# Kernel tuning notes

Hardware: AMD Instinct MI355X
Metric: run time of the kernel (lower is better)

Reference implementation:

```python
import jax, jax.numpy as jnp
import numpy as np
import math

H = 8        # n_heads
FACTOR = 5   # ProbSparse factor


def layer_norm(x, g, b, eps=1e-5):
    m = x.mean(-1, keepdims=True)
    v = ((x - m) ** 2).mean(-1, keepdims=True)
    return (x - m) / jnp.sqrt(v + eps) * g + b


def conv1d_circular(x, w, b=None):
    # x: [B, L, Cin], w: [Cout, Cin, 3]; Conv1d(k=3, padding=1, padding_mode='circular')
    xp = jnp.concatenate([x[:, -1:], x, x[:, :1]], axis=1)
    y = jax.lax.conv_general_dilated(xp.transpose(0, 2, 1), w, (1,), 'VALID',
                                     dimension_numbers=('NCH', 'OIH', 'NCH'))
    if b is not None:
        y = y + b[None, :, None]
    return y.transpose(0, 2, 1)


def pos_encoding(L, d):
    pos = jnp.arange(L, dtype=jnp.float32)[:, None]
    div = jnp.exp(jnp.arange(0, d, 2, dtype=jnp.float32) * (-math.log(10000.0) / d))
    pe = jnp.zeros((L, d), dtype=jnp.float32)
    pe = pe.at[:, 0::2].set(jnp.sin(pos * div))
    pe = pe.at[:, 1::2].set(jnp.cos(pos * div))
    return pe


def prob_attention(rng, Q, K, V):
    # Q, K, V: [B, H, L, E]; non-causal ProbSparse self-attention (mask_flag=False)
    B, Hh, L, E = Q.shape
    c = FACTOR * int(np.ceil(np.log(L)))
    U_part = min(c, L)  # sampled keys per query (sparsity measurement)
    u = min(c, L)       # number of active (top) queries
    idx = jax.random.randint(rng, (L, U_part), 0, L)          # shared over B,H as in torch
    K_sample = K[:, :, idx]                                   # [B,H,L,U,E] gather
    QK_sample = jnp.einsum('bhle,bhlue->bhlu', Q, K_sample)
    M = QK_sample.max(-1) - QK_sample.sum(-1) / L             # sparsity score per query
    M_top = jax.lax.top_k(M, u)[1]                            # [B,H,u] active query ids
    Q_red = jnp.take_along_axis(Q, M_top[..., None], axis=2)  # [B,H,u,E]
    scores = jnp.einsum('bhue,bhle->bhul', Q_red, K) * (1.0 / math.sqrt(E))
    attn = jax.nn.softmax(scores, axis=-1)
    upd = jnp.einsum('bhul,bhle->bhue', attn, V)
    # initial context: mean of V for every query; overwrite active queries
    ctx = jnp.broadcast_to(V.mean(axis=2, keepdims=True), (B, Hh, L, E))
    bi = jnp.arange(B)[:, None, None]
    hi = jnp.arange(Hh)[None, :, None]
    ctx = ctx.at[bi, hi, M_top].set(upd)
    return ctx.transpose(0, 2, 1, 3)  # [B,L,H,E]


def encoder_layer(rng, x, Wq, bq, Wk, bk, Wv, bv, Wo, bo, g1, b1, w1, bf1, w2, bf2, g2, b2):
    B, L, D = x.shape
    dh = D // H
    q = (x @ Wq.T + bq).reshape(B, L, H, dh).transpose(0, 2, 1, 3)
    k = (x @ Wk.T + bk).reshape(B, L, H, dh).transpose(0, 2, 1, 3)
    v = (x @ Wv.T + bv).reshape(B, L, H, dh).transpose(0, 2, 1, 3)
    o = prob_attention(rng, q, k, v).reshape(B, L, D)
    x = x + (o @ Wo.T + bo)            # dropout is identity in eval
    x = layer_norm(x, g1, b1)
    y = jax.nn.gelu(x @ w1.T + bf1, approximate=False)  # conv1 k=1 == linear
    y = y @ w2.T + bf2
    return layer_norm(x + y, g2, b2)


def conv_distill(x, w, b, bg, bb):
    # Conv1d(circular,k=3) -> BatchNorm1d(eval: mean 0, var 1) -> ELU -> MaxPool1d(3,2,1)
    y = conv1d_circular(x, w, b)
    y = y / math.sqrt(1.0 + 1e-5) * bg + bb
    y = jax.nn.elu(y)
    yc = jnp.pad(y.transpose(0, 2, 1), ((0, 0), (0, 0), (1, 1)), constant_values=-jnp.inf)
    p = jax.lax.reduce_window(yc, -jnp.inf, jax.lax.max, (1, 1, 3), (1, 1, 2), 'VALID')
    return p.transpose(0, 2, 1)  # [B, L//2, D]


def forward(x_enc, emb_w, Wq, bq, Wk, bk, Wv, bv, Wo, bo, ln1_g, ln1_b, ff_w1, ff_b1, ff_w2, ff_b2, ln2_g, ln2_b, cv_w, cv_b, bn_g, bn_b, norm_g, norm_b):
    B, L, _ = x_enc.shape
    D = emb_w.shape[0]
    x = conv1d_circular(x_enc, emb_w) + pos_encoding(L, D)[None]  # GazeEmbedding
    base = jax.random.key(42)
    EL = Wq.shape[0]
    for i in range(EL):
        rng = jax.random.fold_in(base, i)
        x = encoder_layer(rng, x, Wq[i], bq[i], Wk[i], bk[i], Wv[i], bv[i], Wo[i], bo[i],
                          ln1_g[i], ln1_b[i], ff_w1[i], ff_b1[i], ff_w2[i], ff_b2[i], ln2_g[i], ln2_b[i])
        if i < EL - 1:
            x = conv_distill(x, cv_w[i], cv_b[i], bn_g[i], bn_b[i])
    return layer_norm(x, norm_g, norm_b)


def setup_inputs() -> dict:
    key = jax.random.key(0)
    ks = jax.random.split(key, 16)
    B, L, C, D, F, EL = 4, 2048, 2, 512, 512, 3
    s = 0.02
    return {
        'x_enc': jax.random.normal(ks[0], (B, L, C), jnp.float32),
        'emb_w': jax.random.normal(ks[1], (D, C, 3), jnp.float32) * s,
        'Wq': jax.random.normal(ks[2], (EL, D, D), jnp.float32) * s,
        'bq': jnp.zeros((EL, D), jnp.float32),
        'Wk': jax.random.normal(ks[3], (EL, D, D), jnp.float32) * s,
        'bk': jnp.zeros((EL, D), jnp.float32),
        'Wv': jax.random.normal(ks[4], (EL, D, D), jnp.float32) * s,
        'bv': jnp.zeros((EL, D), jnp.float32),
        'Wo': jax.random.normal(ks[5], (EL, D, D), jnp.float32) * s,
        'bo': jnp.zeros((EL, D), jnp.float32),
        'ln1_g': jnp.ones((EL, D), jnp.float32),
        'ln1_b': jnp.zeros((EL, D), jnp.float32),
        'ff_w1': jax.random.normal(ks[6], (EL, F, D), jnp.float32) * s,
        'ff_b1': jnp.zeros((EL, F), jnp.float32),
        'ff_w2': jax.random.normal(ks[7], (EL, D, F), jnp.float32) * s,
        'ff_b2': jnp.zeros((EL, D), jnp.float32),
        'ln2_g': jnp.ones((EL, D), jnp.float32),
        'ln2_b': jnp.zeros((EL, D), jnp.float32),
        'cv_w': jax.random.normal(ks[8], (EL - 1, D, D, 3), jnp.float32) * s,
        'cv_b': jnp.zeros((EL - 1, D), jnp.float32),
        'bn_g': jnp.ones((EL - 1, D), jnp.float32),
        'bn_b': jnp.zeros((EL - 1, D), jnp.float32),
        'norm_g': jnp.ones((D,), jnp.float32),
        'norm_b': jnp.zeros((D,), jnp.float32),
    }


def reference(x_enc, emb_w, Wq, bq, Wk, bk, Wv, bv, Wo, bo, ln1_g, ln1_b, ff_w1, ff_b1, ff_w2, ff_b2, ln2_g, ln2_b, cv_w, cv_b, bn_g, bn_b, norm_g, norm_b):
    return forward(x_enc, emb_w, Wq, bq, Wk, bk, Wv, bv, Wo, bo, ln1_g, ln1_b, ff_w1, ff_b1, ff_w2, ff_b2, ln2_g, ln2_b, cv_w, cv_b, bn_g, bn_b, norm_g, norm_b)
```

## Files before the change

### kernel.cpp

```cpp
#include <hip/hip_runtime.h>
#include <cmath>
#include <cstdint>

#define D_MODEL 512
#define NH 8
#define DH 64

static inline int ceil_div(int a, int b) { return (a + b - 1) / b; }

typedef __attribute__((ext_vector_type(8))) short short8;
typedef __attribute__((ext_vector_type(4))) float floatx4;

__device__ __forceinline__ unsigned short f2bf(float f) {
  uint32_t u = __float_as_uint(f);
  uint32_t r = (u + 0x7fffu + ((u >> 16) & 1u)) >> 16;
  return (unsigned short)r;
}
__device__ __forceinline__ float bf2f(unsigned short s) {
  return __uint_as_float(((uint32_t)s) << 16);
}

#define TF_ROTL(x, r) (((x) << (r)) | ((x) >> (32 - (r))))

__host__ __device__ inline void threefry2x32(uint32_t k0, uint32_t k1,
                                             uint32_t x0, uint32_t x1,
                                             uint32_t* o0, uint32_t* o1) {
  uint32_t ks2 = k0 ^ k1 ^ 0x1BD11BDAu;
  x0 += k0; x1 += k1;
#define TF_R4(a, b, c, d)                                    \
  x0 += x1; x1 = TF_ROTL(x1, a); x1 ^= x0;                   \
  x0 += x1; x1 = TF_ROTL(x1, b); x1 ^= x0;                   \
  x0 += x1; x1 = TF_ROTL(x1, c); x1 ^= x0;                   \
  x0 += x1; x1 = TF_ROTL(x1, d); x1 ^= x0;
  TF_R4(13, 15, 26, 6);  x0 += k1;  x1 += ks2 + 1u;
  TF_R4(17, 29, 16, 24); x0 += ks2; x1 += k0 + 2u;
  TF_R4(13, 15, 26, 6);  x0 += k0;  x1 += k1 + 3u;
  TF_R4(17, 29, 16, 24); x0 += k1;  x1 += ks2 + 4u;
  TF_R4(13, 15, 26, 6);  x0 += ks2; x1 += k0 + 5u;
#undef TF_R4
  *o0 = x0; *o1 = x1;
}

__global__ __launch_bounds__(256) void cast3_qkv_kernel(
    const float* __restrict__ s0, const float* __restrict__ s1,
    const float* __restrict__ s2, unsigned short* __restrict__ dst) {
  int sel = blockIdx.x / 768, bb = blockIdx.x % 768;
  int i = (bb * 256 + threadIdx.x) * 4;
  const float* s = (sel == 0) ? s0 : (sel == 1) ? s1 : s2;
  float4 v = *(const float4*)(s + i);
  ushort4 o;
  o.x = f2bf(v.x); o.y = f2bf(v.y); o.z = f2bf(v.z); o.w = f2bf(v.w);
  int layer = i >> 18, off = i & 262143;
  *(ushort4*)(dst + (size_t)layer * 786432 + sel * 262144 + off) = o;
}

__global__ __launch_bounds__(256) void cast3_flat_kernel(
    const float* __restrict__ s0, const float* __restrict__ s1,
    const float* __restrict__ s2, unsigned short* __restrict__ dst) {
  int sel = blockIdx.x / 768, bb = blockIdx.x % 768;
  int i = (bb * 256 + threadIdx.x) * 4;
  const float* s = (sel == 0) ? s0 : (sel == 1) ? s1 : s2;
  float4 v = *(const float4*)(s + i);
  ushort4 o;
  o.x = f2bf(v.x); o.y = f2bf(v.y); o.z = f2bf(v.z); o.w = f2bf(v.w);
  *(ushort4*)(dst + (size_t)sel * 786432 + i) = o;
}

__global__ __launch_bounds__(256) void cast_cvperm_kernel(
    const float* __restrict__ src, unsigned short* __restrict__ dst) {
  int o = blockIdx.x * 256 + threadIdx.x;
  int m = o / 786432, rem = o % 786432;
  int n = rem / 1536, q = rem % 1536;
  int k = q >> 9, c = q & 511;
  dst[o] = f2bf(src[(size_t)m * 786432 + n * 1536 + c * 3 + k]);
}

__global__ __launch_bounds__(256) void embed_kernel(
    const float* __restrict__ x_enc, const float* __restrict__ emb_w,
    float* __restrict__ x, unsigned short* __restrict__ xb, int B, int L) {
  int i = blockIdx.x * 256 + threadIdx.x;
  int total = B * L * D_MODEL;
  if (i >= total) return;
  int d = i % D_MODEL;
  int l = (i / D_MODEL) % L;
  int b = i / (D_MODEL * L);
  int lm = (l == 0) ? (L - 1) : (l - 1);
  int lp = (l == L - 1) ? 0 : (l + 1);
  const float* w = emb_w + d * 6;
  const float* xb_in = x_enc + (size_t)b * L * 2;
  float acc = 0.f;
  acc += xb_in[lm * 2 + 0] * w[0] + xb_in[l * 2 + 0] * w[1] + xb_in[lp * 2 + 0] * w[2];
  acc += xb_in[lm * 2 + 1] * w[3] + xb_in[l * 2 + 1] * w[4] + xb_in[lp * 2 + 1] * w[5];
  int j = d >> 1;
  const float coef = -0.017988946039015985f;
  float div = expf((float)(2 * j) * coef);
  float ang = (float)l * div;
  float pe = (d & 1) ? cosf(ang) : sinf(ang);
  float v = acc + pe;
  x[i] = v;
  xb[i] = f2bf(v);
}

__global__ __launch_bounds__(256) void ln_kernel(
    const float* __restrict__ in, const float* __restrict__ g,
    const float* __restrict__ b, float* __restrict__ out) {
  int row = blockIdx.x;
  int t = threadIdx.x;
  const float* xr = in + (size_t)row * D_MODEL;
  float v0 = xr[t], v1 = xr[t + 256];
  __shared__ float red[256];
  red[t] = v0 + v1;
  __syncthreads();
  for (int s = 128; s > 0; s >>= 1) { if (t < s) red[t] += red[t + s]; __syncthreads(); }
  float mean = red[0] * (1.0f / 512.0f);
  __syncthreads();
  float d0 = v0 - mean, d1 = v1 - mean;
  red[t] = d0 * d0 + d1 * d1;
  __syncthreads();
  for (int s = 128; s > 0; s >>= 1) { if (t < s) red[t] += red[t + s]; __syncthreads(); }
  float var = red[0] * (1.0f / 512.0f);
  float rstd = 1.0f / sqrtf(var + 1e-5f);
  float* outr = out + (size_t)row * D_MODEL;
  outr[t]       = d0 * rstd * g[t]       + b[t];
  outr[t + 256] = d1 * rstd * g[t + 256] + b[t + 256];
}

__global__ __launch_bounds__(256) void ln_dual_kernel(
    const float* __restrict__ in, const float* __restrict__ g,
    const float* __restrict__ b, float* __restrict__ out,
    unsigned short* __restrict__ out16) {
  int row = blockIdx.x;
  int t = threadIdx.x;
  const float* xr = in + (size_t)row * D_MODEL;
  float v0 = xr[t], v1 = xr[t + 256];
  __shared__ float red[256];
  red[t] = v0 + v1;
  __syncthreads();
  for (int s = 128; s > 0; s >>= 1) { if (t < s) red[t] += red[t + s]; __syncthreads(); }
  float mean = red[0] * (1.0f / 512.0f);
  __syncthreads();
  float d0 = v0 - mean, d1 = v1 - mean;
  red[t] = d0 * d0 + d1 * d1;
  __syncthreads();
  for (int s = 128; s > 0; s >>= 1) { if (t < s) red[t] += red[t + s]; __syncthreads(); }
  float var = red[0] * (1.0f / 512.0f);
  float rstd = 1.0f / sqrtf(var + 1e-5f);
  float* outr = out + (size_t)row * D_MODEL;
  unsigned short* o16 = out16 + (size_t)row * D_MODEL;
  float r0 = d0 * rstd * g[t] + b[t];
  float r1 = d1 * rstd * g[t + 256] + b[t + 256];
  outr[t] = r0;       o16[t] = f2bf(r0);
  outr[t + 256] = r1; o16[t + 256] = f2bf(r1);
}

__device__ __forceinline__ float epilogue_apply(int MODE, float v, float r,
                                                float g, float bb, float scl) {
  if (MODE == 1) {
    v = 0.5f * v * (1.0f + erff(v * 0.7071067811865475f));
  } else if (MODE == 2) {
    v += r;
  } else if (MODE == 3) {
    v = v * scl * g + bb;
    v = (v > 0.f) ? v : expm1f(v);
  }
  return v;
}


__device__ __forceinline__ void gload16(const void* g, void* l) {
  __builtin_amdgcn_global_load_lds(
      (const __attribute__((address_space(1))) unsigned int*)g,
      (__attribute__((address_space(3))) unsigned int*)l, 16, 0, 0);
}

__device__ __forceinline__ int xcd_swz(int orig, int nwg) {
  int q = nwg >> 3, r = nwg & 7;
  int x = orig & 7, o = orig >> 3;
  return (x < r ? x * (q + 1) : r * (q + 1) + (x - r) * q) + o;
}

__device__ __forceinline__ void stage64(const unsigned short* __restrict__ G,
                                        int ldk, int row0, int k0,
                                        unsigned short* lds, int tid) {
  const int wave = tid >> 6;
#pragma unroll
  for (int iss = 0; iss < 2; ++iss) {
    int s = iss * 256 + tid;
    int r = s >> 3;
    int cs = (s & 7) ^ (r & 7);
    gload16(G + (size_t)(row0 + r) * ldk + k0 + cs * 8,
            lds + (size_t)(iss * 256 + wave * 64) * 8);
  }
}

__device__ __forceinline__ short8 frag64(const unsigned short* t, int row,
                                         int chunk) {
  return *(const short8*)(t + row * 64 + ((chunk ^ (row & 7)) * 8));
}

struct Acc4 { floatx4 v[2][2]; };

__device__ __forceinline__ void gemm64_core(
    const unsigned short* __restrict__ A, int lda,
    const unsigned short* __restrict__ Bt, int ldb, int K, int bm, int bn,
    unsigned short* lds , int tid, Acc4& out) {
  const int wave = tid >> 6, lane = tid & 63;
  const int wm = (wave >> 1) * 32, wn = (wave & 1) * 32;
  const int quad = lane >> 4, l16 = lane & 15;
  floatx4 z = {0.f, 0.f, 0.f, 0.f};
  floatx4 a00 = z, a01 = z, a10 = z, a11 = z;
  stage64(A, lda, bm, 0, lds, tid);
  stage64(Bt, ldb, bn, 0, lds + 4096, tid);
  __syncthreads();
  const int nk = K >> 6;
  for (int t = 0; t < nk; ++t) {
    const int cur = (t & 1) * 8192;
    if (t + 1 < nk) {
      const int nxt = 8192 - cur;
      stage64(A, lda, bm, (t + 1) << 6, lds + nxt, tid);
      stage64(Bt, ldb, bn, (t + 1) << 6, lds + nxt + 4096, tid);
    }
    const unsigned short* At = lds + cur;
    const unsigned short* Bl = lds + cur + 4096;
#pragma unroll
    for (int ks = 0; ks < 2; ++ks) {
      short8 f0 = frag64(At, wm + l16,      ks * 4 + quad);
      short8 f1 = frag64(At, wm + 16 + l16, ks * 4 + quad);
      short8 g0 = frag64(Bl, wn + l16,      ks * 4 + quad);
      short8 g1 = frag64(Bl, wn + 16 + l16, ks * 4 + quad);
      a00 = __builtin_amdgcn_mfma_f32_16x16x32_bf16(f0, g0, a00, 0, 0, 0);
      a01 = __builtin_amdgcn_mfma_f32_16x16x32_bf16(f0, g1, a01, 0, 0, 0);
      a10 = __builtin_amdgcn_mfma_f32_16x16x32_bf16(f1, g0, a10, 0, 0, 0);
      a11 = __builtin_amdgcn_mfma_f32_16x16x32_bf16(f1, g1, a11, 0, 0, 0);
    }
    __syncthreads();
  }
  out.v[0][0] = a00; out.v[0][1] = a01; out.v[1][0] = a10; out.v[1][1] = a11;
}

template <int MODE, int OUT>
__global__ __launch_bounds__(256) void bgemm_kernel(
    const unsigned short* __restrict__ A, const unsigned short* __restrict__ Bt,
    const float* __restrict__ bias, const float* __restrict__ R,
    const float* __restrict__ gvec, const float* __restrict__ bvec,
    float* __restrict__ C, unsigned short* __restrict__ C16,
    int M, int N, int K, float scl) {
  __shared__ unsigned short lds[16384];
  const int tid = threadIdx.x;
  const int gridN = N >> 6;
  const int wgid = xcd_swz(blockIdx.x, (int)gridDim.x);
  const int bn = (wgid % gridN) * 64;
  const int bm = (wgid / gridN) * 64;
  Acc4 acc;
  gemm64_core(A, K, Bt, K, K, bm, bn, lds, tid, acc);
  const int wave = tid >> 6, lane = tid & 63;
  const int wm = (wave >> 1) * 32, wn = (wave & 1) * 32;
  const int quad = lane >> 4, l16 = lane & 15;
#pragma unroll
  for (int i = 0; i < 2; ++i) {
#pragma unroll
    for (int j = 0; j < 2; ++j) {
      int col = bn + wn + j * 16 + l16;
#pragma unroll
      for (int p = 0; p < 4; ++p) {
        int row = bm + wm + i * 16 + quad * 4 + p;
        float v = acc.v[i][j][p] + bias[col];
        v = epilogue_apply(MODE, v, (MODE == 2) ? R[(size_t)row * N + col] : 0.f,
                           (MODE == 3) ? gvec[col] : 0.f,
                           (MODE == 3) ? bvec[col] : 0.f, scl);
        if (OUT & 1) C[(size_t)row * N + col] = v;
        if (OUT & 2) C16[(size_t)row * N + col] = f2bf(v);
      }
    }
  }
}

template <int MODE, int OUT>
static void run_bgemm(const unsigned short* A, const unsigned short* Bt,
                      const float* bias, const float* R, const float* g,
                      const float* bb, float* C, unsigned short* C16,
                      int M, int N, int K, float scl, hipStream_t stream) {
  int nwg = (N / 64) * (M / 64);
  bgemm_kernel<MODE, OUT><<<nwg, 256, 0, stream>>>(A, Bt, bias, R, g, bb, C,
                                                   C16, M, N, K, scl);
}

__global__ __launch_bounds__(256) void qkv_gemm_kernel(
    const unsigned short* __restrict__ A, const unsigned short* __restrict__ Bt,
    const float* __restrict__ bqp, const float* __restrict__ bkp,
    const float* __restrict__ bvp, float* __restrict__ Cq,
    float* __restrict__ Cv, unsigned short* __restrict__ K16o, int M, int K) {
  __shared__ unsigned short lds[16384];
  const int tid = threadIdx.x;
  const int gridN = 24;
  const int wgid = xcd_swz(blockIdx.x, (int)gridDim.x);
  const int bn = (wgid % gridN) * 64;
  const int bm = (wgid / gridN) * 64;
  Acc4 acc;
  gemm64_core(A, K, Bt, K, K, bm, bn, lds, tid, acc);
  const int wave = tid >> 6, lane = tid & 63;
  const int wm = (wave >> 1) * 32, wn = (wave & 1) * 32;
  const int quad = lane >> 4, l16 = lane & 15;
#pragma unroll
  for (int i = 0; i < 2; ++i) {
#pragma unroll
    for (int j = 0; j < 2; ++j) {
      int col = bn + wn + j * 16 + l16;
      int seg = col >> 9, nn = col & 511;
      const float* bp = (seg == 0) ? bqp : (seg == 1) ? bkp : bvp;
      float bsv = bp[nn];
#pragma unroll
      for (int p = 0; p < 4; ++p) {
        int row = bm + wm + i * 16 + quad * 4 + p;
        float v = acc.v[i][j][p] + bsv;
        if (seg == 1) {
          K16o[(size_t)row * 512 + nn] = f2bf(v);
        } else {
          float* Cd = (seg == 0) ? Cq : Cv;
          Cd[(size_t)row * 512 + nn] = v;
        }
      }
    }
  }
}

__global__ __launch_bounds__(256) void conv_gemm_kernel(
    const unsigned short* __restrict__ Axl, const unsigned short* __restrict__ Bt,
    const float* __restrict__ bias, const float* __restrict__ gvec,
    const float* __restrict__ bvec, float* __restrict__ C,
    int M, int L, int log2L, float scl) {
  __shared__ unsigned short lds[16384];
  const int tid = threadIdx.x;
  const int wgid = xcd_swz(blockIdx.x, (int)gridDim.x);
  const int bn = (wgid & 7) * 64;
  const int bm = (wgid >> 3) * 64;
  const int wave = tid >> 6, lane = tid & 63;
  const int wm = (wave >> 1) * 32, wn = (wave & 1) * 32;
  const int quad = lane >> 4, l16 = lane & 15;
  floatx4 z = {0.f, 0.f, 0.f, 0.f};
  floatx4 a00 = z, a01 = z, a10 = z, a11 = z;

#define STAGE_A_CONV(T, DST)                                               \
  {                                                                        \
    _Pragma("unroll") for (int iss = 0; iss < 2; ++iss) {                  \
      int s = iss * 256 + tid;                                             \
      int r = s >> 3;                                                      \
      int cs = (s & 7) ^ (r & 7);                                          \
      int row = bm + r;                                                    \
      int li = row & (L - 1);                                              \
      int bb2 = row >> log2L;                                              \
      int l2 = (li + ((T) >> 3) - 1 + L) & (L - 1);                        \
      gload16(Axl + (((size_t)((bb2 << log2L) + l2)) << 9) +               \
                  (((T) & 7) << 6) + cs * 8,                               \
              (DST) + (size_t)(iss * 256 + wave * 64) * 8);                \
    }                                                                      \
  }

  STAGE_A_CONV(0, lds);
  stage64(Bt, 1536, bn, 0, lds + 4096, tid);
  __syncthreads();
  for (int t = 0; t < 24; ++t) {
    const int cur = (t & 1) * 8192;
    if (t + 1 < 24) {
      const int nxt = 8192 - cur;
      STAGE_A_CONV(t + 1, lds + nxt);
      stage64(Bt, 1536, bn, (t + 1) << 6, lds + nxt + 4096, tid);
    }
    const unsigned short* At = lds + cur;
    const unsigned short* Bl = lds + cur + 4096;
#pragma unroll
    for (int ks = 0; ks < 2; ++ks) {
      short8 f0 = frag64(At, wm + l16,      ks * 4 + quad);
      short8 f1 = frag64(At, wm + 16 + l16, ks * 4 + quad);
      short8 g0 = frag64(Bl, wn + l16,      ks * 4 + quad);
      short8 g1 = frag64(Bl, wn + 16 + l16, ks * 4 + quad);
      a00 = __builtin_amdgcn_mfma_f32_16x16x32_bf16(f0, g0, a00, 0, 0, 0);
      a01 = __builtin_amdgcn_mfma_f32_16x16x32_bf16(f0, g1, a01, 0, 0, 0);
      a10 = __builtin_amdgcn_mfma_f32_16x16x32_bf16(f1, g0, a10, 0, 0, 0);
      a11 = __builtin_amdgcn_mfma_f32_16x16x32_bf16(f1, g1, a11, 0, 0, 0);
    }
    __syncthreads();
  }
#undef STAGE_A_CONV
  floatx4 accs[2][2] = {{a00, a01}, {a10, a11}};
#pragma unroll
  for (int i = 0; i < 2; ++i) {
#pragma unroll
    for (int j = 0; j < 2; ++j) {
      int col = bn + wn + j * 16 + l16;
      float gv = gvec[col], bbv = bvec[col], bsv = bias[col];
#pragma unroll
      for (int p = 0; p < 4; ++p) {
        int row = bm + wm + i * 16 + quad * 4 + p;
        float v = accs[i][j][p] + bsv;
        v = epilogue_apply(3, v, 0.f, gv, bbv, scl);
        C[(size_t)row * 512 + col] = v;
      }
    }
  }
}

__global__ __launch_bounds__(256) void sparse_qk_fused_kernel(
    const float* __restrict__ Q, const unsigned short* __restrict__ K16,
    float* __restrict__ Mout, int B, int L, int U, uint32_t k0, uint32_t k1) {
  __shared__ int idxl[64];
  __shared__ float wmax[4][8];
  __shared__ float wsum[4][8];
  int bl = blockIdx.x;
  int b = bl / L, l = bl - b * L;
  int tid = threadIdx.x;
  int wave = tid >> 6, lane = tid & 63;
  if (tid < U) {
    uint32_t o0, o1;
    threefry2x32(k0, k1, 0u, (uint32_t)(l * U + tid), &o0, &o1);
    idxl[tid] = (int)((o0 ^ o1) & (uint32_t)(L - 1));
  }
  int h = lane >> 3;
  const float4* qr = (const float4*)(Q + (size_t)bl * D_MODEL + lane * 8);
  float4 q0 = qr[0], q1 = qr[1];
  float qv[8] = {q0.x, q0.y, q0.z, q0.w, q1.x, q1.y, q1.z, q1.w};
  __syncthreads();
  float mx = -INFINITY, sm = 0.f;
  for (int u = wave; u < U; u += 4) {
    int ki = idxl[u];
    short8 k8 = *(const short8*)(K16 + ((size_t)b * L + ki) * D_MODEL + lane * 8);
    float p = 0.f;
#pragma unroll
    for (int e = 0; e < 8; ++e) p += qv[e] * bf2f((unsigned short)k8[e]);
    p += __shfl_xor(p, 1);
    p += __shfl_xor(p, 2);
    p += __shfl_xor(p, 4);
    mx = fmaxf(mx, p);
    sm += p;
  }
  if ((lane & 7) == 0) { wmax[wave][h] = mx; wsum[wave][h] = sm; }
  __syncthreads();
  if (tid < 8) {
    float m = fmaxf(fmaxf(wmax[0][tid], wmax[1][tid]),
                    fmaxf(wmax[2][tid], wmax[3][tid]));
    float s = wsum[0][tid] + wsum[1][tid] + wsum[2][tid] + wsum[3][tid];
    Mout[((size_t)(b * NH + tid)) * L + l] = m - s / (float)L;
  }
}

template <int NE>
__global__ __launch_bounds__(256) void topk_kernel(
    const float* __restrict__ Mv, const float* __restrict__ Q,
    int* __restrict__ Mtop, unsigned int* __restrict__ bmap,
    unsigned short* __restrict__ qred16, float* __restrict__ vmean,
    int words, int u, int L) {
  int bh = blockIdx.x;
  int b = bh >> 3, h = bh & 7;
  int t = threadIdx.x;
  int wave = t >> 6, lane = t & 63;
  const int base = wave * 64 * NE;
  const float* src = Mv + (size_t)bh * (NE * 256);
  uint32_t ov[NE];
#pragma unroll
  for (int i = 0; i < NE; ++i) {
    uint32_t bits = __float_as_uint(src[base + i * 64 + lane]);
    uint32_t m = (uint32_t)((int32_t)bits >> 31) | 0x80000000u;
    ov[i] = bits ^ m;
  }
  if (t < words) bmap[bh * words + t] = 0u;
  if (t < 64) vmean[bh * 64 + t] = 0.f;

  uint32_t T = 0;
  for (int bit = 31; bit >= 0; --bit) {
    uint32_t cand = T | (1u << bit);
    int c = 0;
#pragma unroll
    for (int i = 0; i < NE; ++i)
      c += (int)__popcll(__ballot(ov[i] >= cand));
    if (c >= u) T = cand;
  }
  int c_gt = 0;
#pragma unroll
  for (int i = 0; i < NE; ++i)
    c_gt += (int)__popcll(__ballot(ov[i] > T));
  int need = u - c_gt;
  int I = 0;
  for (int bit = 10; bit >= 0; --bit) {
    int cand = I | (1 << bit);
    int c = 0;
#pragma unroll
    for (int i = 0; i < NE; ++i)
      c += (int)__popcll(__ballot(ov[i] == T && (base + i * 64 + lane) < cand));
    if (c < need) I = cand;
  }
  __shared__ uint32_t kOrd[160];
  __shared__ int kIdx[160];
  __shared__ int smTop[40];
  int cnt_pre = 0;
#pragma unroll
  for (int i = 0; i < NE; ++i) {
    int ix = base + i * 64 + lane;
    bool sel = (ov[i] > T) || (ov[i] == T && ix <= I);
    unsigned long long bal = __ballot(sel);
    if (sel) {
      int pos = wave * u + cnt_pre +
                (int)__popcll(bal & ((1ull << lane) - 1ull));
      kOrd[pos] = ov[i];
      kIdx[pos] = ix;
    }
    cnt_pre += (int)__popcll(bal);
  }
  __syncthreads();
  int total = 4 * u;
  if (t < total) {
    uint32_t myo = kOrd[t];
    int myi = kIdx[t];
    int rank = 0;
    for (int j = 0; j < total; ++j) {
      uint32_t jo = kOrd[j];
      int ji = kIdx[j];
      rank += (jo > myo || (jo == myo && ji < myi)) ? 1 : 0;
    }
    if (rank < u) {
      Mtop[bh * u + rank] = myi;
      smTop[rank] = myi;
      atomicOr(&bmap[bh * words + (myi >> 5)], 1u << (myi & 31));
    }
  }
  __syncthreads();
  int d = t & 63;
  for (int r = t >> 6; r < 64; r += 4) {
    float v = 0.f;
    if (r < u) {
      int l = smTop[r];
      v = Q[((size_t)(b * L + l)) * D_MODEL + h * DH + d];
    }
    qred16[((size_t)bh * 64 + r) * 64 + d] = f2bf(v);
  }
}

static void run_topk(const float* Mv, const float* Q, int* Mtop,
                     unsigned int* bmap, unsigned short* qred16, float* vmean,
                     int L, int u, hipStream_t stream) {
  int words = L / 32;
  if (L == 2048)
    topk_kernel<8><<<32, 256, 0, stream>>>(Mv, Q, Mtop, bmap, qred16, vmean, words, u, L);
  else if (L == 1024)
    topk_kernel<4><<<32, 256, 0, stream>>>(Mv, Q, Mtop, bmap, qred16, vmean, words, u, L);
  else
    topk_kernel<2><<<32, 256, 0, stream>>>(Mv, Q, Mtop, bmap, qred16, vmean, words, u, L);
}

__global__ __launch_bounds__(256) void vmean_partial_kernel(
    const float* __restrict__ V, float* __restrict__ vmean, int L) {
  int b = blockIdx.y;
  int chunk = blockIdx.x;
  int rows = L >> 6;
  int t = threadIdx.x;
  const float* base = V + ((size_t)b * L + (size_t)chunk * rows) * D_MODEL;
  float s0 = 0.f, s1 = 0.f;
  for (int r = 0; r < rows; ++r) {
    s0 += base[(size_t)r * D_MODEL + t];
    s1 += base[(size_t)r * D_MODEL + t + 256];
  }
  float invL = 1.0f / (float)L;
  atomicAdd(&vmean[b * D_MODEL + t], s0 * invL);
  atomicAdd(&vmean[b * D_MODEL + t + 256], s1 * invL);
}

__global__ void fill_ctx_kernel(const float* __restrict__ vmean,
                                const unsigned int* __restrict__ bmap,
                                unsigned short* __restrict__ O16,
                                float* __restrict__ O32, int B, int L,
                                int words) {
  int i = blockIdx.x * 256 + threadIdx.x;
  int total = B * L * D_MODEL;
  if (i >= total) return;
  int dcol = i % D_MODEL;
  int l = (i / D_MODEL) % L;
  int b = i / (D_MODEL * L);
  int h = dcol >> 6;
  unsigned int w = bmap[(b * NH + h) * words + (l >> 5)];
  bool sel = (w >> (l & 31)) & 1u;
  O16[i] = f2bf(sel ? 0.f : vmean[b * D_MODEL + dcol]);
  if (sel) O32[i] = 0.f;
}

__global__ void cast_sel_kernel(const float* __restrict__ O32,
                                const int* __restrict__ Mtop,
                                unsigned short* __restrict__ O16, int L,
                                int U) {
  int z = blockIdx.x;
  int b = z >> 3, h = z & 7;
  int t = threadIdx.x;
  int d = t & 63;
  for (int r = t >> 6; r < U; r += 4) {
    int l = Mtop[z * U + r];
    size_t off = ((size_t)(b * L + l)) * D_MODEL + h * DH + d;
    O16[off] = f2bf(O32[off]);
  }
}

__global__ __launch_bounds__(256) void scores_mfma_kernel(
    const unsigned short* __restrict__ qred16,
    const unsigned short* __restrict__ k16, float* __restrict__ S, int L) {
  __shared__ unsigned short lds[16384];
  const int z = blockIdx.y;
  const int b = z >> 3, h = z & 7;
  const int bn = blockIdx.x * 64;
  const int tid = threadIdx.x;
  Acc4 acc;
  gemm64_core(qred16 + (size_t)z * 4096, 64,
              k16 + (size_t)b * L * D_MODEL + h * DH, D_MODEL, 64, 0, bn, lds,
              tid, acc);
  float* Sz = S + (size_t)z * 64 * L;
  const int wave = tid >> 6, lane = tid & 63;
  const int wm = (wave >> 1) * 32, wn = (wave & 1) * 32;
  const int quad = lane >> 4, l16 = lane & 15;
#pragma unroll
  for (int i = 0; i < 2; ++i) {
#pragma unroll
    for (int j = 0; j < 2; ++j) {
      int col = bn + wn + j * 16 + l16;
#pragma unroll
      for (int p = 0; p < 4; ++p) {
        int row = wm + i * 16 + quad * 4 + p;
        Sz[(size_t)row * L + col] = 0.125f * acc.v[i][j][p];
      }
    }
  }
}

template <int LC>
__global__ __launch_bounds__(256) void softmax_kernel(float* __restrict__ S,
                                                      int U) {
  constexpr int NE = LC / 256;
  int rid = blockIdx.x;
  int z = rid / U, r = rid % U;
  float* row = S + (size_t)z * 64 * LC + (size_t)r * LC;
  int t = threadIdx.x;
  float vals[NE];
  float m = -INFINITY;
#pragma unroll
  for (int i = 0; i < NE; ++i) {
    vals[i] = row[t + i * 256];
    m = fmaxf(m, vals[i]);
  }
  __shared__ float red[256];
  red[t] = m;
  __syncthreads();
  for (int s = 128; s > 0; s >>= 1) { if (t < s) red[t] = fmaxf(red[t], red[t + s]); __syncthreads(); }
  m = red[0];
  __syncthreads();
  float sum = 0.f;
#pragma unroll
  for (int i = 0; i < NE; ++i) {
    vals[i] = expf(vals[i] - m);
    sum += vals[i];
  }
  red[t] = sum;
  __syncthreads();
  for (int s = 128; s > 0; s >>= 1) { if (t < s) red[t] += red[t + s]; __syncthreads(); }
  float inv = 1.0f / red[0];
#pragma unroll
  for (int i = 0; i < NE; ++i) row[t + i * 256] = vals[i] * inv;
}

static void run_softmax(float* S, int L, int U, hipStream_t stream) {
  int blocks = 32 * U;
  if (L == 2048)      softmax_kernel<2048><<<blocks, 256, 0, stream>>>(S, U);
  else if (L == 1024) softmax_kernel<1024><<<blocks, 256, 0, stream>>>(S, U);
  else                softmax_kernel<512><<<blocks, 256, 0, stream>>>(S, U);
}

#define PV_LC 128

template <int U>
__global__ __launch_bounds__(256) void pv_kernel(
    const float* __restrict__ P, const float* __restrict__ V,
    const int* __restrict__ Mtop, float* __restrict__ O, int L) {
  __shared__ float Pl[U][PV_LC];
  __shared__ float Vl[PV_LC][DH + 4];
  const int z = blockIdx.y;
  const int b = z / NH, h = z % NH;
  const int c0 = blockIdx.x * PV_LC;
  const int tid = threadIdx.x;
  const float* Pz = P + (size_t)z * 64 * L + c0;
  for (int i4 = tid; i4 < U * (PV_LC / 4); i4 += 256) {
    int r = i4 / (PV_LC / 4);
    int lq = (i4 % (PV_LC / 4)) * 4;
    float4 p4 = *(const float4*)(Pz + (size_t)r * L + lq);
    Pl[r][lq + 0] = p4.x; Pl[r][lq + 1] = p4.y;
    Pl[r][lq + 2] = p4.z; Pl[r][lq + 3] = p4.w;
  }
  const float* Vb = V + ((size_t)b * L + c0) * D_MODEL + h * DH;
  for (int i4 = tid; i4 < PV_LC * (DH / 4); i4 += 256) {
    int l = i4 >> 4;
    int d4 = (i4 & 15) * 4;
    float4 v4 = *(const float4*)(Vb + (size_t)l * D_MODEL + d4);
    Vl[l][d4 + 0] = v4.x; Vl[l][d4 + 1] = v4.y;
    Vl[l][d4 + 2] = v4.z; Vl[l][d4 + 3] = v4.w;
  }
  __syncthreads();
  const int wave = tid >> 6, lane = tid & 63;
  constexpr int NJ = (U + 3) / 4;
  float acc[NJ] = {};
  for (int l = 0; l < PV_LC; ++l) {
    float vv = Vl[l][lane];
#pragma unroll
    for (int j = 0; j < NJ; ++j) {
      int r = wave + 4 * j;
      if (r < U) acc[j] += Pl[r][l] * vv;
    }
  }
#pragma unroll
  for (int j = 0; j < NJ; ++j) {
    int r = wave + 4 * j;
    if (r < U) {
      int ml = Mtop[z * U + r];
      atomicAdd(&O[((size_t)(b * L + ml)) * D_MODEL + h * DH + lane], acc[j]);
    }
  }
}

static void run_pv(const float* P, const float* V, const int* Mtop, float* O,
                   int L, int U, hipStream_t stream) {
  dim3 gg(L / PV_LC, 32);
  if (U == 40)      pv_kernel<40><<<gg, 256, 0, stream>>>(P, V, Mtop, O, L);
  else if (U == 35) pv_kernel<35><<<gg, 256, 0, stream>>>(P, V, Mtop, O, L);
  else              pv_kernel<64><<<gg, 256, 0, stream>>>(P, V, Mtop, O, L);
}

__global__ void maxpool_kernel(const float* __restrict__ Y,
                               float* __restrict__ X,
                               unsigned short* __restrict__ Xb, int B, int L) {
  int Lo = L / 2;
  int i = blockIdx.x * 256 + threadIdx.x;
  int total = B * Lo * D_MODEL;
  if (i >= total) return;
  int d = i % D_MODEL;
  int lp = (i / D_MODEL) % Lo;
  int b = i / (D_MODEL * Lo);
  int l0 = 2 * lp - 1;
  float m = -INFINITY;
#pragma unroll
  for (int k = 0; k < 3; ++k) {
    int l = l0 + k;
    if (l >= 0 && l < L) m = fmaxf(m, Y[((size_t)(b * L + l)) * D_MODEL + d]);
  }
  X[i] = m;
  Xb[i] = f2bf(m);
}

extern "C" void kernel_launch(void* const* d_in, const int* in_sizes, int n_in,
                              void* d_out, int out_size, void* d_ws,
                              size_t ws_size, hipStream_t stream) {
  const float* x_enc  = (const float*)d_in[0];
  const float* emb_w  = (const float*)d_in[1];
  const float* Wq     = (const float*)d_in[2];
  const float* bq     = (const float*)d_in[3];
  const float* Wk     = (const float*)d_in[4];
  const float* bk     = (const float*)d_in[5];
  const float* Wv     = (const float*)d_in[6];
  const float* bv     = (const float*)d_in[7];
  const float* Wo     = (const float*)d_in[8];
  const float* bo     = (const float*)d_in[9];
  const float* ln1_g  = (const float*)d_in[10];
  const float* ln1_b  = (const float*)d_in[11];
  const float* ff_w1  = (const float*)d_in[12];
  const float* ff_b1  = (const float*)d_in[13];
  const float* ff_w2  = (const float*)d_in[14];
  const float* ff_b2  = (const float*)d_in[15];
  const float* ln2_g  = (const float*)d_in[16];
  const float* ln2_b  = (const float*)d_in[17];
  const float* cv_w   = (const float*)d_in[18];
  const float* cv_b   = (const float*)d_in[19];
  const float* bn_g   = (const float*)d_in[20];
  const float* bn_b   = (const float*)d_in[21];
  const float* norm_g = (const float*)d_in[22];
  const float* norm_b = (const float*)d_in[23];

  const int B = 4, L0 = 2048, EL = 3;
  const size_t SZ = (size_t)B * 2048 * 512;
  float* ws   = (float*)d_ws;
  float* xbuf = ws;
  float* ebuf = ws + SZ;
  float* qbuf = ws + 2 * SZ;
  float* kbuf = ws + 3 * SZ;
  float* vbuf = ws + 4 * SZ;
  float* obuf = ws + 5 * SZ;
  float* sm   = ws + 6 * SZ;
  float*         d_M     = sm;
  int*           d_Mtop  = (int*)(sm + 65536);
  float*         d_vmean = sm + 65536 + 1280;
  unsigned int*  d_bmap  = (unsigned int*)(sm + 65536 + 1280 + 2048);
  unsigned short* qred16 = (unsigned short*)(sm + 65536 + 1280 + 2048 + 2048);
  unsigned short* wgt  = (unsigned short*)(ws + 6 * SZ + 160000);
  unsigned short* qkvw = wgt;
  unsigned short* wof  = wgt + 3 * 786432;
  unsigned short* wow  = wof;
  unsigned short* w1w  = wof + 786432;
  unsigned short* w2w  = wof + 2 * 786432;
  unsigned short* cvw2 = wof + 3 * 786432;

  float* Sbuf = ebuf;
  const float inv_s = 1.0f / sqrtf(1.0f + 1e-5f);

  cast3_qkv_kernel<<<3 * 768, 256, 0, stream>>>(Wq, Wk, Wv, qkvw);
  cast3_flat_kernel<<<3 * 768, 256, 0, stream>>>(Wo, ff_w1, ff_w2, wof);
  cast_cvperm_kernel<<<6144, 256, 0, stream>>>(cv_w, cvw2);

  embed_kernel<<<ceil_div(B * L0 * D_MODEL, 256), 256, 0, stream>>>(
      x_enc, emb_w, xbuf, (unsigned short*)ebuf, B, L0);
  unsigned short* xb16 = (unsigned short*)ebuf;

  int L = L0;
  int log2L = 11;
  for (int i = 0; i < EL; ++i) {
    const int M_ = B * L;
    int c = 5 * (int)ceil(log((double)L));
    int U = c < L ? c : L;
    int words = L / 32;
    unsigned short* k16 = (unsigned short*)kbuf;

    qkv_gemm_kernel<<<24 * (M_ / 64), 256, 0, stream>>>(
        xb16, qkvw + (size_t)i * 786432, bq + i * 512, bk + i * 512,
        bv + i * 512, qbuf, vbuf, k16, M_, 512);

    uint32_t lk0, lk1, k20, k21;
    threefry2x32(0u, 42u, 0u, (uint32_t)i, &lk0, &lk1);
    threefry2x32(lk0, lk1, 0u, 1u, &k20, &k21);

    sparse_qk_fused_kernel<<<B * L, 256, 0, stream>>>(qbuf, k16, d_M, B, L, U,
                                                      k20, k21);
    run_topk(d_M, qbuf, d_Mtop, d_bmap, qred16, d_vmean, L, U, stream);
    vmean_partial_kernel<<<dim3(64, B), 256, 0, stream>>>(vbuf, d_vmean, L);
    unsigned short* ab16 = (unsigned short*)qbuf;
    fill_ctx_kernel<<<ceil_div(B * L * D_MODEL, 256), 256, 0, stream>>>(
        d_vmean, d_bmap, ab16, obuf, B, L, words);

    scores_mfma_kernel<<<dim3(L / 64, B * NH), 256, 0, stream>>>(qred16, k16,
                                                                 Sbuf, L);
    run_softmax(Sbuf, L, U, stream);
    run_pv(Sbuf, vbuf, d_Mtop, obuf, L, U, stream);
    cast_sel_kernel<<<B * NH, 256, 0, stream>>>(obuf, d_Mtop, ab16, L, U);

    run_bgemm<2, 1>(ab16, wow + (size_t)i * 262144, bo + i * 512, xbuf,
                    nullptr, nullptr, ebuf, nullptr, M_, 512, 512, 0.f,
                    stream);
    ln_dual_kernel<<<M_, 256, 0, stream>>>(ebuf, ln1_g + i * 512,
                                           ln1_b + i * 512, xbuf, ab16);

    unsigned short* ff1b16 = (unsigned short*)obuf;
    run_bgemm<1, 2>(ab16, w1w + (size_t)i * 262144, ff_b1 + i * 512, nullptr,
                    nullptr, nullptr, nullptr, ff1b16, M_, 512, 512, 0.f,
                    stream);
    run_bgemm<2, 1>(ff1b16, w2w + (size_t)i * 262144, ff_b2 + i * 512, xbuf,
                    nullptr, nullptr, ebuf, nullptr, M_, 512, 512, 0.f,
                    stream);

    if (i < EL - 1) {
      unsigned short* xln16 = (unsigned short*)qbuf;
      ln_dual_kernel<<<M_, 256, 0, stream>>>(ebuf, ln2_g + i * 512,
                                             ln2_b + i * 512, xbuf, xln16);
      conv_gemm_kernel<<<8 * (M_ / 64), 256, 0, stream>>>(
          xln16, cvw2 + (size_t)i * 786432, cv_b + i * 512, bn_g + i * 512,
          bn_b + i * 512, ebuf, M_, L, log2L, inv_s);
      xb16 = (unsigned short*)vbuf + 6291456;
      maxpool_kernel<<<ceil_div(B * (L / 2) * D_MODEL, 256), 256, 0, stream>>>(
          ebuf, xbuf, xb16, B, L);
      L /= 2;
      log2L -= 1;
    } else {
      ln_kernel<<<M_, 256, 0, stream>>>(ebuf, ln2_g + i * 512,
                                        ln2_b + i * 512, xbuf);
    }
  }

  ln_kernel<<<B * L, 256, 0, stream>>>(xbuf, norm_g, norm_b, (float*)d_out);
}
```

Before: 695.0 us.

## Use 128x128 GEMM tiles and fold softmax normalization into PV

Adds a 128x128-tile MFMA GEMM core (single-buffered) and uses it for the QKV projection, for large dense GEMMs, and for the circular-conv GEMM when M is large. This raises data reuse per tile and cuts global loads, but gives up the double-buffered prefetch of the 64x64 path and puts more pressure on registers. Separately, softmax no longer writes normalized probabilities back. A stats kernel stores the row max and inverse sum, and the PV kernel applies exp and scaling as it loads scores, removing one full write pass over the score matrix. The scores kernel also skips storing rows beyond U.

After: 744.5 us. +7.1%, slower.

```diff
diff --git a/kernel.cpp b/kernel.cpp
--- a/kernel.cpp
+++ b/kernel.cpp
@@ -193,12 +193,27 @@
   }
 }
 
+__device__ __forceinline__ void stage128(const unsigned short* __restrict__ G,
+                                         int ldk, int row0, int k0,
+                                         unsigned short* lds, int tid) {
+  const int wave = tid >> 6;
+#pragma unroll
+  for (int iss = 0; iss < 4; ++iss) {
+    int s = iss * 256 + tid;
+    int r = s >> 3;
+    int cs = (s & 7) ^ (r & 7);
+    gload16(G + (size_t)(row0 + r) * ldk + k0 + cs * 8,
+            lds + (size_t)(iss * 256 + wave * 64) * 8);
+  }
+}
+
 __device__ __forceinline__ short8 frag64(const unsigned short* t, int row,
                                          int chunk) {
   return *(const short8*)(t + row * 64 + ((chunk ^ (row & 7)) * 8));
 }
 
 struct Acc4 { floatx4 v[2][2]; };
+struct Acc16 { floatx4 v[4][4]; };
 
 __device__ __forceinline__ void gemm64_core(
     const unsigned short* __restrict__ A, int lda,
@@ -236,6 +251,44 @@
     __syncthreads();
   }
   out.v[0][0] = a00; out.v[0][1] = a01; out.v[1][0] = a10; out.v[1][1] = a11;
+}
+
+__device__ __forceinline__ void gemm128_core(
+    const unsigned short* __restrict__ A, int lda,
+    const unsigned short* __restrict__ Bt, int ldb, int K, int bm, int bn,
+    unsigned short* lds , int tid,
+    Acc16& out) {
+  const int wave = tid >> 6, lane = tid & 63;
+  const int wr = (wave >> 1) * 64, wc = (wave & 1) * 64;
+  const int quad = lane >> 4, l16 = lane & 15;
+  floatx4 z = {0.f, 0.f, 0.f, 0.f};
+#pragma unroll
+  for (int a = 0; a < 4; ++a)
+#pragma unroll
+    for (int b = 0; b < 4; ++b) out.v[a][b] = z;
+  const int nk = K >> 6;
+  for (int t = 0; t < nk; ++t) {
+    stage128(A, lda, bm, t << 6, lds, tid);
+    stage128(Bt, ldb, bn, t << 6, lds + 8192, tid);
+    __syncthreads();
+#pragma unroll
+    for (int ks = 0; ks < 2; ++ks) {
+      short8 af[4], bf[4];
+#pragma unroll
+      for (int mi = 0; mi < 4; ++mi)
+        af[mi] = frag64(lds, wr + mi * 16 + l16, ks * 4 + quad);
+#pragma unroll
+      for (int ni = 0; ni < 4; ++ni)
+        bf[ni] = frag64(lds + 8192, wc + ni * 16 + l16, ks * 4 + quad);
+#pragma unroll
+      for (int mi = 0; mi < 4; ++mi)
+#pragma unroll
+        for (int ni = 0; ni < 4; ++ni)
+          out.v[mi][ni] = __builtin_amdgcn_mfma_f32_16x16x32_bf16(
+              af[mi], bf[ni], out.v[mi][ni], 0, 0, 0);
+    }
+    __syncthreads();
+  }
 }
 
 template <int MODE, int OUT>
@@ -276,13 +329,57 @@
 }
 
 template <int MODE, int OUT>
+__global__ __launch_bounds__(256) void bgemm128_kernel(
+    const unsigned short* __restrict__ A, const unsigned short* __restrict__ Bt,
+    const float* __restrict__ bias, const float* __restrict__ R,
+    const float* __restrict__ gvec, const float* __restrict__ bvec,
+    float* __restrict__ C, unsigned short* __restrict__ C16,
+    int M, int N, int K, float scl) {
+  __shared__ unsigned short lds[16384];
+  const int tid = threadIdx.x;
+  const int gridN = N >> 7;
+  const int wgid = xcd_swz(blockIdx.x, (int)gridDim.x);
+  const int bn = (wgid % gridN) * 128;
+  const int bm = (wgid / gridN) * 128;
+  Acc16 acc;
+  gemm128_core(A, K, Bt, K, K, bm, bn, lds, tid, acc);
+  const int wave = tid >> 6, lane = tid & 63;
+  const int wr = (wave >> 1) * 64, wc = (wave & 1) * 64;
+  const int quad = lane >> 4, l16 = lane & 15;
+#pragma unroll
+  for (int mi = 0; mi < 4; ++mi) {
+#pragma unroll
+    for (int ni = 0; ni < 4; ++ni) {
+      int col = bn + wc + ni * 16 + l16;
+#pragma unroll
+      for (int p = 0; p < 4; ++p) {
+        int row = bm + wr + mi * 16 + quad * 4 + p;
+        float v = acc.v[mi][ni][p] + bias[col];
+        v = epilogue_apply(MODE, v, (MODE == 2) ? R[(size_t)row * N + col] : 0.f,
+                           (MODE == 3) ? gvec[col] : 0.f,
+                           (MODE == 3) ? bvec[col] : 0.f, scl);
+        if (OUT & 1) C[(size_t)row * N + col] = v;
+        if (OUT & 2) C16[(size_t)row * N + col] = f2bf(v);
+      }
+    }
+  }
+}
+
+template <int MODE, int OUT>
 static void run_bgemm(const unsigned short* A, const unsigned short* Bt,
                       const float* bias, const float* R, const float* g,
                       const float* bb, float* C, unsigned short* C16,
                       int M, int N, int K, float scl, hipStream_t stream) {
-  int nwg = (N / 64) * (M / 64);
-  bgemm_kernel<MODE, OUT><<<nwg, 256, 0, stream>>>(A, Bt, bias, R, g, bb, C,
-                                                   C16, M, N, K, scl);
+  int n128 = (M >> 7) * (N >> 7);
+  if (n128 >= 192 && (M & 127) == 0 && (N & 127) == 0) {
+    bgemm128_kernel<MODE, OUT><<<n128, 256, 0, stream>>>(A, Bt, bias, R, g,
+                                                         bb, C, C16, M, N, K,
+                                                         scl);
+  } else {
+    int nwg = (N / 64) * (M / 64);
+    bgemm_kernel<MODE, OUT><<<nwg, 256, 0, stream>>>(A, Bt, bias, R, g, bb, C,
+                                                     C16, M, N, K, scl);
+  }
 }
 
 __global__ __launch_bounds__(256) void qkv_gemm_kernel(
@@ -292,33 +389,31 @@
     float* __restrict__ Cv, unsigned short* __restrict__ K16o, int M, int K) {
   __shared__ unsigned short lds[16384];
   const int tid = threadIdx.x;
-  const int gridN = 24;
+  const int gridN = 12;
   const int wgid = xcd_swz(blockIdx.x, (int)gridDim.x);
-  const int bn = (wgid % gridN) * 64;
-  const int bm = (wgid / gridN) * 64;
-  Acc4 acc;
-  gemm64_core(A, K, Bt, K, K, bm, bn, lds, tid, acc);
+  const int bn = (wgid % gridN) * 128;
+  const int bm = (wgid / gridN) * 128;
+  Acc16 acc;
+  gemm128_core(A, K, Bt, K, K, bm, bn, lds, tid, acc);
   const int wave = tid >> 6, lane = tid & 63;
-  const int wm = (wave >> 1) * 32, wn = (wave & 1) * 32;
+  const int wr = (wave >> 1) * 64, wc = (wave & 1) * 64;
   const int quad = lane >> 4, l16 = lane & 15;
-#pragma unroll
-  for (int i = 0; i < 2; ++i) {
-#pragma unroll
-    for (int j = 0; j < 2; ++j) {
-      int col = bn + wn + j * 16 + l16;
-      int seg = col >> 9, nn = col & 511;
-      const float* bp = (seg == 0) ? bqp : (seg == 1) ? bkp : bvp;
+  const int seg = bn >> 9;
+  const float* bp = (seg == 0) ? bqp : (seg == 1) ? bkp : bvp;
+  float* Cd = (seg == 0) ? Cq : Cv;
+#pragma unroll
+  for (int mi = 0; mi < 4; ++mi) {
+#pragma unroll
+    for (int ni = 0; ni < 4; ++ni) {
+      int col = bn + wc + ni * 16 + l16;
+      int nn = col & 511;
       float bsv = bp[nn];
 #pragma unroll
       for (int p = 0; p < 4; ++p) {
-        int row = bm + wm + i * 16 + quad * 4 + p;
-        float v = acc.v[i][j][p] + bsv;
-        if (seg == 1) {
-          K16o[(size_t)row * 512 + nn] = f2bf(v);
-        } else {
-          float* Cd = (seg == 0) ? Cq : Cv;
-          Cd[(size_t)row * 512 + nn] = v;
-        }
+        int row = bm + wr + mi * 16 + quad * 4 + p;
+        float v = acc.v[mi][ni][p] + bsv;
+        if (seg == 1) K16o[(size_t)row * 512 + nn] = f2bf(v);
+        else          Cd[(size_t)row * 512 + nn] = v;
       }
     }
   }
@@ -393,6 +488,82 @@
       for (int p = 0; p < 4; ++p) {
         int row = bm + wm + i * 16 + quad * 4 + p;
         float v = accs[i][j][p] + bsv;
+        v = epilogue_apply(3, v, 0.f, gv, bbv, scl);
+        C[(size_t)row * 512 + col] = v;
+      }
+    }
+  }
+}
+
+__global__ __launch_bounds__(256) void conv_gemm128_kernel(
+    const unsigned short* __restrict__ Axl, const unsigned short* __restrict__ Bt,
+    const float* __restrict__ bias, const float* __restrict__ gvec,
+    const float* __restrict__ bvec, float* __restrict__ C,
+    int M, int L, int log2L, float scl) {
+  __shared__ unsigned short lds[16384];
+  const int tid = threadIdx.x;
+  const int wgid = xcd_swz(blockIdx.x, (int)gridDim.x);
+  const int bn = (wgid & 3) * 128;
+  const int bm = (wgid >> 2) * 128;
+  const int wave = tid >> 6, lane = tid & 63;
+  const int wr = (wave >> 1) * 64, wc = (wave & 1) * 64;
+  const int quad = lane >> 4, l16 = lane & 15;
+  Acc16 acc;
+  floatx4 z = {0.f, 0.f, 0.f, 0.f};
+#pragma unroll
+  for (int a = 0; a < 4; ++a)
+#pragma unroll
+    for (int b = 0; b < 4; ++b) acc.v[a][b] = z;
+
+#define STAGE_A_CONV128(T)                                                 \
+  {                                                                        \
+    _Pragma("unroll") for (int iss = 0; iss < 4; ++iss) {                  \
+      int s = iss * 256 + tid;                                             \
+      int r = s >> 3;                                                      \
+      int cs = (s & 7) ^ (r & 7);                                          \
+      int row = bm + r;                                                    \
+      int li = row & (L - 1);                                              \
+      int bb2 = row >> log2L;                                              \
+      int l2 = (li + ((T) >> 3) - 1 + L) & (L - 1);                        \
+      gload16(Axl + (((size_t)((bb2 << log2L) + l2)) << 9) +               \
+                  (((T) & 7) << 6) + cs * 8,                               \
+              lds + (size_t)(iss * 256 + wave * 64) * 8);                  \
+    }                                                                      \
+  }
+
+  for (int t = 0; t < 24; ++t) {
+    STAGE_A_CONV128(t);
+    stage128(Bt, 1536, bn, t << 6, lds + 8192, tid);
+    __syncthreads();
+#pragma unroll
+    for (int ks = 0; ks < 2; ++ks) {
+      short8 af[4], bf[4];
+#pragma unroll
+      for (int mi = 0; mi < 4; ++mi)
+        af[mi] = frag64(lds, wr + mi * 16 + l16, ks * 4 + quad);
+#pragma unroll
+      for (int ni = 0; ni < 4; ++ni)
+        bf[ni] = frag64(lds + 8192, wc + ni * 16 + l16, ks * 4 + quad);
+#pragma unroll
+      for (int mi = 0; mi < 4; ++mi)
+#pragma unroll
+        for (int ni = 0; ni < 4; ++ni)
+          acc.v[mi][ni] = __builtin_amdgcn_mfma_f32_16x16x32_bf16(
+              af[mi], bf[ni], acc.v[mi][ni], 0, 0, 0);
+    }
+    __syncthreads();
+  }
+#undef STAGE_A_CONV128
+#pragma unroll
+  for (int mi = 0; mi < 4; ++mi) {
+#pragma unroll
+    for (int ni = 0; ni < 4; ++ni) {
+      int col = bn + wc + ni * 16 + l16;
+      float gv = gvec[col], bbv = bvec[col], bsv = bias[col];
+#pragma unroll
+      for (int p = 0; p < 4; ++p) {
+        int row = bm + wr + mi * 16 + quad * 4 + p;
+        float v = acc.v[mi][ni][p] + bsv;
         v = epilogue_apply(3, v, 0.f, gv, bbv, scl);
         C[(size_t)row * 512 + col] = v;
       }
@@ -598,7 +769,8 @@
 
 __global__ __launch_bounds__(256) void scores_mfma_kernel(
     const unsigned short* __restrict__ qred16,
-    const unsigned short* __restrict__ k16, float* __restrict__ S, int L) {
+    const unsigned short* __restrict__ k16, float* __restrict__ S, int L,
+    int U) {
   __shared__ unsigned short lds[16384];
   const int z = blockIdx.y;
   const int b = z >> 3, h = z & 7;
@@ -620,19 +792,20 @@
 #pragma unroll
       for (int p = 0; p < 4; ++p) {
         int row = wm + i * 16 + quad * 4 + p;
-        Sz[(size_t)row * L + col] = 0.125f * acc.v[i][j][p];
+        if (row < U) Sz[(size_t)row * L + col] = 0.125f * acc.v[i][j][p];
       }
     }
   }
 }
 
 template <int LC>
-__global__ __launch_bounds__(256) void softmax_kernel(float* __restrict__ S,
-                                                      int U) {
+__global__ __launch_bounds__(256) void softmax_stats_kernel(
+    const float* __restrict__ S, float* __restrict__ mrow,
+    float* __restrict__ lrow, int U) {
   constexpr int NE = LC / 256;
   int rid = blockIdx.x;
   int z = rid / U, r = rid % U;
-  float* row = S + (size_t)z * 64 * LC + (size_t)r * LC;
+  const float* row = S + (size_t)z * 64 * LC + (size_t)r * LC;
   int t = threadIdx.x;
   float vals[NE];
   float m = -INFINITY;
@@ -649,23 +822,22 @@
   __syncthreads();
   float sum = 0.f;
 #pragma unroll
-  for (int i = 0; i < NE; ++i) {
-    vals[i] = expf(vals[i] - m);
-    sum += vals[i];
-  }
+  for (int i = 0; i < NE; ++i) sum += expf(vals[i] - m);
   red[t] = sum;
   __syncthreads();
   for (int s = 128; s > 0; s >>= 1) { if (t < s) red[t] += red[t + s]; __syncthreads(); }
-  float inv = 1.0f / red[0];
-#pragma unroll
-  for (int i = 0; i < NE; ++i) row[t + i * 256] = vals[i] * inv;
-}
-
-static void run_softmax(float* S, int L, int U, hipStream_t stream) {
+  if (t == 0) {
+    mrow[z * 64 + r] = m;
+    lrow[z * 64 + r] = 1.0f / red[0];
+  }
+}
+
+static void run_stats(const float* S, float* mrow, float* lrow, int L, int U,
+                      hipStream_t stream) {
   int blocks = 32 * U;
-  if (L == 2048)      softmax_kernel<2048><<<blocks, 256, 0, stream>>>(S, U);
-  else if (L == 1024) softmax_kernel<1024><<<blocks, 256, 0, stream>>>(S, U);
-  else                softmax_kernel<512><<<blocks, 256, 0, stream>>>(S, U);
+  if (L == 2048)      softmax_stats_kernel<2048><<<blocks, 256, 0, stream>>>(S, mrow, lrow, U);
+  else if (L == 1024) softmax_stats_kernel<1024><<<blocks, 256, 0, stream>>>(S, mrow, lrow, U);
+  else                softmax_stats_kernel<512><<<blocks, 256, 0, stream>>>(S, mrow, lrow, U);
 }
 
 #define PV_LC 128
@@ -673,20 +845,27 @@
 template <int U>
 __global__ __launch_bounds__(256) void pv_kernel(
     const float* __restrict__ P, const float* __restrict__ V,
+    const float* __restrict__ mrow, const float* __restrict__ lrow,
     const int* __restrict__ Mtop, float* __restrict__ O, int L) {
   __shared__ float Pl[U][PV_LC];
   __shared__ float Vl[PV_LC][DH + 4];
+  __shared__ float Msh[U], Ish[U];
   const int z = blockIdx.y;
   const int b = z / NH, h = z % NH;
   const int c0 = blockIdx.x * PV_LC;
   const int tid = threadIdx.x;
+  if (tid < U) { Msh[tid] = mrow[z * 64 + tid]; Ish[tid] = lrow[z * 64 + tid]; }
+  __syncthreads();
   const float* Pz = P + (size_t)z * 64 * L + c0;
   for (int i4 = tid; i4 < U * (PV_LC / 4); i4 += 256) {
     int r = i4 / (PV_LC / 4);
     int lq = (i4 % (PV_LC / 4)) * 4;
     float4 p4 = *(const float4*)(Pz + (size_t)r * L + lq);
-    Pl[r][lq + 0] = p4.x; Pl[r][lq + 1] = p4.y;
-    Pl[r][lq + 2] = p4.z; Pl[r][lq + 3] = p4.w;
+    float mr = Msh[r], ir = Ish[r];
+    Pl[r][lq + 0] = expf(p4.x - mr) * ir;
+    Pl[r][lq + 1] = expf(p4.y - mr) * ir;
+    Pl[r][lq + 2] = expf(p4.z - mr) * ir;
+    Pl[r][lq + 3] = expf(p4.w - mr) * ir;
   }
   const float* Vb = V + ((size_t)b * L + c0) * D_MODEL + h * DH;
   for (int i4 = tid; i4 < PV_LC * (DH / 4); i4 += 256) {
@@ -718,12 +897,13 @@
   }
 }
 
-static void run_pv(const float* P, const float* V, const int* Mtop, float* O,
-                   int L, int U, hipStream_t stream) {
+static void run_pv(const float* P, const float* V, const float* mrow,
+                   const float* lrow, const int* Mtop, float* O, int L, int U,
+                   hipStream_t stream) {
   dim3 gg(L / PV_LC, 32);
-  if (U == 40)      pv_kernel<40><<<gg, 256, 0, stream>>>(P, V, Mtop, O, L);
-  else if (U == 35) pv_kernel<35><<<gg, 256, 0, stream>>>(P, V, Mtop, O, L);
-  else              pv_kernel<64><<<gg, 256, 0, stream>>>(P, V, Mtop, O, L);
+  if (U == 40)      pv_kernel<40><<<gg, 256, 0, stream>>>(P, V, mrow, lrow, Mtop, O, L);
+  else if (U == 35) pv_kernel<35><<<gg, 256, 0, stream>>>(P, V, mrow, lrow, Mtop, O, L);
+  else              pv_kernel<64><<<gg, 256, 0, stream>>>(P, V, mrow, lrow, Mtop, O, L);
 }
 
 __global__ void maxpool_kernel(const float* __restrict__ Y,
@@ -790,6 +970,8 @@
   float*         d_vmean = sm + 65536 + 1280;
   unsigned int*  d_bmap  = (unsigned int*)(sm + 65536 + 1280 + 2048);
   unsigned short* qred16 = (unsigned short*)(sm + 65536 + 1280 + 2048 + 2048);
+  float*         d_mrow  = sm + 136448;
+  float*         d_lrow  = sm + 138496;
   unsigned short* wgt  = (unsigned short*)(ws + 6 * SZ + 160000);
   unsigned short* qkvw = wgt;
   unsigned short* wof  = wgt + 3 * 786432;
@@ -818,7 +1000,7 @@
     int words = L / 32;
     unsigned short* k16 = (unsigned short*)kbuf;
 
-    qkv_gemm_kernel<<<24 * (M_ / 64), 256, 0, stream>>>(
+    qkv_gemm_kernel<<<12 * (M_ / 128), 256, 0, stream>>>(
         xb16, qkvw + (size_t)i * 786432, bq + i * 512, bk + i * 512,
         bv + i * 512, qbuf, vbuf, k16, M_, 512);
 
@@ -835,9 +1017,9 @@
         d_vmean, d_bmap, ab16, obuf, B, L, words);
 
     scores_mfma_kernel<<<dim3(L / 64, B * NH), 256, 0, stream>>>(qred16, k16,
-                                                                 Sbuf, L);
-    run_softmax(Sbuf, L, U, stream);
-    run_pv(Sbuf, vbuf, d_Mtop, obuf, L, U, stream);
+                                                                 Sbuf, L, U);
+    run_stats(Sbuf, d_mrow, d_lrow, L, U, stream);
+    run_pv(Sbuf, vbuf, d_mrow, d_lrow, d_Mtop, obuf, L, U, stream);
     cast_sel_kernel<<<B * NH, 256, 0, stream>>>(obuf, d_Mtop, ab16, L, U);
 
     run_bgemm<2, 1>(ab16, wow + (size_t)i * 262144, bo + i * 512, xbuf,
@@ -858,9 +1040,15 @@
       unsigned short* xln16 = (unsigned short*)qbuf;
       ln_dual_kernel<<<M_, 256, 0, stream>>>(ebuf, ln2_g + i * 512,
                                              ln2_b + i * 512, xbuf, xln16);
-      conv_gemm_kernel<<<8 * (M_ / 64), 256, 0, stream>>>(
-          xln16, cvw2 + (size_t)i * 786432, cv_b + i * 512, bn_g + i * 512,
-          bn_b + i * 512, ebuf, M_, L, log2L, inv_s);
+      if (M_ >= 8192) {
+        conv_gemm128_kernel<<<4 * (M_ / 128), 256, 0, stream>>>(
+            xln16, cvw2 + (size_t)i * 786432, cv_b + i * 512, bn_g + i * 512,
+            bn_b + i * 512, ebuf, M_, L, log2L, inv_s);
+      } else {
+        conv_gemm_kernel<<<8 * (M_ / 64), 256, 0, stream>>>(
+            xln16, cvw2 + (size_t)i * 786432, cv_b + i * 512, bn_g + i * 512,
+            bn_b + i * 512, ebuf, M_, L, log2L, inv_s);
+      }
       xb16 = (unsigned short*)vbuf + 6291456;
       maxpool_kernel<<<ceil_div(B * (L / 2) * D_MODEL, 256), 256, 0, stream>>>(
           ebuf, xbuf, xb16, B, L);
```
